# Performance work log

Measured on AMD Instinct MI355X. Metric: run time of the kernel, lower is better.

## Reference

```python
import jax, jax.numpy as jnp
import numpy as np


def setup_inputs() -> dict:
    key = jax.random.key(0)
    k1, k2 = jax.random.split(key)
    B, T, D = 16, 512, 256
    feats = jax.random.normal(k1, (B, T, D), dtype=jnp.float32)
    hidden = jax.random.normal(k2, (B, T, 2 * D), dtype=jnp.float32)
    return {"feats": feats, "hidden": hidden, "seq_len": T}


def reference(feats, hidden, seq_len):
    # feats: (B, T, D); hidden: (B, T, 2D); all sequences have length seq_len == T
    B, T, D = feats.shape
    zero = jnp.zeros((B, 1, D), dtype=feats.dtype)
    # X_fw layout per sequence: [feat_0..feat_{T-1}, 0]; X_bw: [0, feat_0..feat_{T-1}]
    X_fw = jnp.concatenate([feats, zero], axis=1).reshape(B * (T + 1), D)
    X_bw = jnp.concatenate([zero, feats], axis=1).reshape(B * (T + 1), D)

    h_fw = hidden[..., :D]  # (B, T, D) forward LSTM half
    h_bw = hidden[..., D:]  # (B, T, D) backward LSTM half

    # (B, T, N) with N = B*(T+1): full softmax over every token slot (as original)
    fw_lp = jax.nn.log_softmax(jnp.einsum('btd,nd->btn', h_fw, X_fw), axis=-1)
    bw_lp = jax.nn.log_softmax(jnp.einsum('btd,nd->btn', h_bw, X_bw), axis=-1)

    t = jnp.arange(T)
    # original takes diag of columns [1:1+T] (fw) and [0:T] (bw) for EVERY sequence
    fw_diag = fw_lp[:, t, t + 1]  # (B, T)
    bw_diag = bw_lp[:, t, t]      # (B, T)

    fw_loss = (-fw_diag.sum(axis=1) / seq_len).sum() / B
    bw_loss = (-bw_diag.sum(axis=1) / seq_len).sum() / B
    return fw_loss, bw_loss
```

## Files before the change

### kernel.cpp

```cpp
#include <hip/hip_runtime.h>
#include <hip/hip_bf16.h>
#include <stdint.h>

typedef int   int32x4 __attribute__((ext_vector_type(4)));
typedef float floatx4 __attribute__((ext_vector_type(4)));

#define D      256
#define TLEN   512
#define BATCH  16
#define NQ     16384
#define NK     8192
#define BN     64
#define KS     16
#define NTILE  (NK / BN)
#define TPS    (NTILE / KS)
#define TILE_BYTES (BN * D)
#define MSHIFT 64.0f
#define QSCALE 32.0f
#define SSCALE 11818.5577f
#define SMAGIC 1065095716.0f
#define LOG2E  1.4426950408889634f

__device__ __forceinline__ int q8(float x) {
    float y = x * QSCALE;
    y = fminf(fmaxf(y, -127.f), 127.f);
    return (int)rintf(y);
}

__device__ __forceinline__ void quant16(const float* __restrict__ src,
                                        int32x4* __restrict__ dst, int i) {
    const float4* s4 = reinterpret_cast<const float4*>(src) + (size_t)i * 4;
    int32x4 o;
    #pragma unroll
    for (int j = 0; j < 4; ++j) {
        float4 v = s4[j];
        o[j] = (q8(v.x) & 255) | ((q8(v.y) & 255) << 8) |
               ((q8(v.z) & 255) << 16) | ((q8(v.w) & 255) << 24);
    }
    dst[i] = o;
}

__global__ void prep_kernel(const float* __restrict__ feats,
                            const float* __restrict__ hidden,
                            int32x4* __restrict__ Qi8, int32x4* __restrict__ Ki8,
                            float* __restrict__ tfw, float* __restrict__ tbw) {
    int b = blockIdx.x;
    if (b < 1024) {
        quant16(hidden, Qi8, b * 256 + threadIdx.x);
        return;
    }
    if (b < 1536) {
        quant16(feats, Ki8, (b - 1024) * 256 + threadIdx.x);
        return;
    }
    int gw   = (b - 1536) * 4 + (threadIdx.x >> 6);
    int lane = threadIdx.x & 63;
    int t = gw & (TLEN - 1);
    const float4* h4 = reinterpret_cast<const float4*>(hidden + (size_t)gw * (2 * D));
    float sfw = 0.f, sbw = 0.f;
    if (t < TLEN - 1) {
        const float4* f4 = reinterpret_cast<const float4*>(feats + (size_t)(t + 1) * D);
        float4 x = h4[lane], y = f4[lane];
        sfw = x.x * y.x + x.y * y.y + x.z * y.z + x.w * y.w;
    }
    if (t > 0) {
        const float4* f4 = reinterpret_cast<const float4*>(feats + (size_t)(t - 1) * D);
        float4 x = h4[64 + lane], y = f4[lane];
        sbw = x.x * y.x + x.y * y.y + x.z * y.z + x.w * y.w;
    }
    #pragma unroll
    for (int mask = 32; mask > 0; mask >>= 1) {
        sfw += __shfl_xor(sfw, mask);
        sbw += __shfl_xor(sbw, mask);
    }
    if (lane == 0) { tfw[gw] = sfw; tbw[gw] = sbw; }
}

__global__ __launch_bounds__(512, 2) void lse_kernel(const char* __restrict__ Qi8,
                                                     const char* __restrict__ Ki8,
                                                     float* __restrict__ ps) {
    const int qblk  = blockIdx.x >> 4;
    const int slice = blockIdx.x & 15;
    const int q0    = qblk * 512;
    const int tid   = threadIdx.x;
    const int wave  = tid >> 6;
    const int lane  = tid & 63;
    const int lrow  = lane & 15;
    const int lgrp  = lane >> 4;

    __shared__ __align__(16) char Klds[2][BN * D];

    int32x4 a[4][4];
    #pragma unroll
    for (int mf = 0; mf < 4; ++mf) {
        const char* qbase = Qi8 + (size_t)(q0 + wave * 64 + mf * 16 + lrow) * D + lgrp * 16;
        #pragma unroll
        for (int s = 0; s < 4; ++s)
            a[mf][s] = *reinterpret_cast<const int32x4*>(qbase + s * 64);
    }

    int voff[4];
    #pragma unroll
    for (int s = 0; s < 4; ++s)
        voff[s] = lrow * 256 + ((((s * 4 + lgrp) ^ (lrow & 7))) * 16);

    int soff[2];
    #pragma unroll
    for (int i = 0; i < 2; ++i) {
        int cl  = tid + i * 512;
        int row = cl >> 4, c = cl & 15;
        soff[i] = (row * 16 + (c ^ (row & 7))) * 16;
    }

    const char* ksrc = Ki8 + (size_t)(slice * TPS) * TILE_BYTES;

    auto issue = [&](int buf, int t) {
        const char* tb = ksrc + (size_t)t * TILE_BYTES;
        #pragma unroll
        for (int i = 0; i < 2; ++i) {
            const char* gp = tb + soff[i];
            char* lp = (char*)(&Klds[0][0]) + buf * 16384 + (i * 512 + wave * 64) * 16;
            __builtin_amdgcn_global_load_lds(
                (const __attribute__((address_space(1))) void*)gp,
                (__attribute__((address_space(3))) void*)lp,
                16, 0, 0);
        }
    };

    float srun[4][4];
    #pragma unroll
    for (int mf = 0; mf < 4; ++mf)
        #pragma unroll
        for (int r = 0; r < 4; ++r) srun[mf][r] = 0.f;

    auto compute = [&](int buf) {
        const char* kb = (const char*)(&Klds[0][0]) + buf * 16384;
        #pragma unroll
        for (int sub = 0; sub < 4; ++sub) {
            int32x4 c[4];
            #pragma unroll
            for (int mf = 0; mf < 4; ++mf)
                c[mf] = (int32x4){-65536, -65536, -65536, -65536};
            __builtin_amdgcn_s_setprio(1);
            #pragma unroll
            for (int s = 0; s < 4; ++s) {
                int32x4 bfr = *reinterpret_cast<const int32x4*>(kb + voff[s] + sub * 4096);
                #pragma unroll
                for (int mf = 0; mf < 4; ++mf)
                    c[mf] = __builtin_amdgcn_mfma_i32_16x16x64_i8(a[mf][s], bfr, c[mf], 0, 0, 0);
            }
            __builtin_amdgcn_s_setprio(0);
            #pragma unroll
            for (int mf = 0; mf < 4; ++mf)
                #pragma unroll
                for (int r = 0; r < 4; ++r) {
                    float f = (float)c[mf][r];
                    float tt = fmaf(f, SSCALE, SMAGIC);
                    uint32_t u = (uint32_t)tt;
                    srun[mf][r] += __uint_as_float(u);
                }
        }
    };

    issue(0, 0);

    #pragma unroll 1
    for (int t = 0; t < TPS; t += 2) {
        asm volatile("s_waitcnt vmcnt(0)" ::: "memory");
        __builtin_amdgcn_s_barrier();
        asm volatile("" ::: "memory");
        issue(1, t + 1);
        compute(0);
        asm volatile("s_waitcnt vmcnt(0)" ::: "memory");
        __builtin_amdgcn_s_barrier();
        asm volatile("" ::: "memory");
        if (t + 2 < TPS) issue(0, t + 2);
        compute(1);
    }

    #pragma unroll
    for (int mf = 0; mf < 4; ++mf)
        #pragma unroll
        for (int r = 0; r < 4; ++r) {
            float v = srun[mf][r];
            v += __shfl_xor(v, 1);
            v += __shfl_xor(v, 2);
            v += __shfl_xor(v, 4);
            v += __shfl_xor(v, 8);
            if (lrow == 0) {
                int q = q0 + wave * 64 + mf * 16 + lgrp * 4 + r;
                ps[slice * NQ + q] = v;
            }
        }
}

__global__ void reduce1_kernel(const float* __restrict__ ps,
                               const float* __restrict__ tfw, const float* __restrict__ tbw,
                               float* __restrict__ partial) {
    __shared__ float red0[256], red1[256];
    int tid = threadIdx.x;
    int i   = blockIdx.x * 256 + tid;
    const float Z16 = 16.f * __expf(-MSHIFT);
    int qf = 2 * i, qb = 2 * i + 1;
    float sfw = Z16, sbw = Z16;
    #pragma unroll
    for (int sl = 0; sl < KS; ++sl) {
        sfw += ps[sl * NQ + qf];
        sbw += ps[sl * NQ + qb];
    }
    float lsef = MSHIFT + logf(sfw);
    float lseb = MSHIFT + logf(sbw);
    red0[tid] = lsef - tfw[i];
    red1[tid] = lseb - tbw[i];
    __syncthreads();
    for (int s2 = 128; s2 > 0; s2 >>= 1) {
        if (tid < s2) { red0[tid] += red0[tid + s2]; red1[tid] += red1[tid + s2]; }
        __syncthreads();
    }
    if (tid == 0) {
        partial[blockIdx.x * 2 + 0] = red0[0];
        partial[blockIdx.x * 2 + 1] = red1[0];
    }
}

__global__ void reduce2_kernel(const float* __restrict__ partial, float* __restrict__ out) {
    int lane = threadIdx.x & 63;
    float fw = (lane < 32) ? partial[lane * 2 + 0] : 0.f;
    float bw = (lane < 32) ? partial[lane * 2 + 1] : 0.f;
    #pragma unroll
    for (int mask = 32; mask > 0; mask >>= 1) {
        fw += __shfl_xor(fw, mask);
        bw += __shfl_xor(bw, mask);
    }
    if (lane == 0) {
        const float denom = (float)TLEN * (float)BATCH;
        out[0] = fw / denom;
        out[1] = bw / denom;
    }
}

extern "C" void kernel_launch(void* const* d_in, const int* in_sizes, int n_in,
                              void* d_out, int out_size, void* d_ws, size_t ws_size,
                              hipStream_t stream) {
    const float* feats  = (const float*)d_in[0];
    const float* hidden = (const float*)d_in[1];
    float* out = (float*)d_out;

    char* ws = (char*)d_ws;
    char*  Qi8  = ws;
    char*  Ki8  = ws + (size_t)NQ * D;
    float* psv  = (float*)(ws + (size_t)NQ * D + (size_t)NK * D);
    float* tfw  = psv + (size_t)KS * NQ;
    float* tbw  = tfw + NK;
    float* part = tbw + NK;

    prep_kernel<<<3584, 256, 0, stream>>>(feats, hidden,
                                          (int32x4*)Qi8, (int32x4*)Ki8, tfw, tbw);

    lse_kernel<<<(NQ / 512) * KS, 512, 0, stream>>>(Qi8, Ki8, psv);

    reduce1_kernel<<<NK / 256, 256, 0, stream>>>(psv, tfw, tbw, part);
    reduce2_kernel<<<1, 64, 0, stream>>>(part, out);
}
```

Baseline: 61.37 us.

## Load int8 key fragments directly from global into registers, dropping LDS staging

The LSE kernel no longer stages key tiles through double-buffered LDS with global_load_lds and barriers. Each wave now loads its B-fragments straight from global memory into two register sets, prefetching the next subtile while the current one runs MFMAs. Blocks shrink to 256 threads and block IDs are remapped across slices. The exp2 bit trick also switches from a biased accumulator init to a new magic constant clamped at zero. The intent is to remove LDS traffic and barrier stalls, at the cost of redundant per-wave global/L2 reads of the same keys.

```diff
diff --git a/kernel.cpp b/kernel.cpp
--- a/kernel.cpp
+++ b/kernel.cpp
@@ -3,23 +3,19 @@
 #include <stdint.h>
 
 typedef int   int32x4 __attribute__((ext_vector_type(4)));
-typedef float floatx4 __attribute__((ext_vector_type(4)));
 
 #define D      256
 #define TLEN   512
 #define BATCH  16
 #define NQ     16384
 #define NK     8192
-#define BN     64
 #define KS     16
-#define NTILE  (NK / BN)
-#define TPS    (NTILE / KS)
-#define TILE_BYTES (BN * D)
+#define SLICE_KEYS (NK / KS)
+#define NSUB   (SLICE_KEYS / 16)
 #define MSHIFT 64.0f
 #define QSCALE 32.0f
-#define SSCALE 11818.5577f
-#define SMAGIC 1065095716.0f
-#define LOG2E  1.4426950408889634f
+#define SSCALE  11818.5577749f
+#define SMAGIC2 290554713.0f
 
 __device__ __forceinline__ int q8(float x) {
     float y = x * QSCALE;
@@ -76,19 +72,18 @@
     if (lane == 0) { tfw[gw] = sfw; tbw[gw] = sbw; }
 }
 
-__global__ __launch_bounds__(512, 2) void lse_kernel(const char* __restrict__ Qi8,
-                                                     const char* __restrict__ Ki8,
-                                                     float* __restrict__ ps) {
-    const int qblk  = blockIdx.x >> 4;
-    const int slice = blockIdx.x & 15;
-    const int q0    = qblk * 512;
-    const int tid   = threadIdx.x;
-    const int wave  = tid >> 6;
-    const int lane  = tid & 63;
+__global__ __launch_bounds__(256) void lse_kernel(const char* __restrict__ Qi8,
+                                                  const char* __restrict__ Ki8,
+                                                  float* __restrict__ ps) {
+    const int bid   = (int)blockIdx.x;
+    const int nbid  = (bid & 7) * 128 + (bid >> 3);
+    const int slice = nbid >> 6;
+    const int qblk  = nbid & 63;
+    const int q0    = qblk * 256;
+    const int wave  = (int)(threadIdx.x >> 6);
+    const int lane  = (int)(threadIdx.x & 63);
     const int lrow  = lane & 15;
     const int lgrp  = lane >> 4;
-
-    __shared__ __align__(16) char Klds[2][BN * D];
 
     int32x4 a[4][4];
     #pragma unroll
@@ -99,33 +94,7 @@
             a[mf][s] = *reinterpret_cast<const int32x4*>(qbase + s * 64);
     }
 
-    int voff[4];
-    #pragma unroll
-    for (int s = 0; s < 4; ++s)
-        voff[s] = lrow * 256 + ((((s * 4 + lgrp) ^ (lrow & 7))) * 16);
-
-    int soff[2];
-    #pragma unroll
-    for (int i = 0; i < 2; ++i) {
-        int cl  = tid + i * 512;
-        int row = cl >> 4, c = cl & 15;
-        soff[i] = (row * 16 + (c ^ (row & 7))) * 16;
-    }
-
-    const char* ksrc = Ki8 + (size_t)(slice * TPS) * TILE_BYTES;
-
-    auto issue = [&](int buf, int t) {
-        const char* tb = ksrc + (size_t)t * TILE_BYTES;
-        #pragma unroll
-        for (int i = 0; i < 2; ++i) {
-            const char* gp = tb + soff[i];
-            char* lp = (char*)(&Klds[0][0]) + buf * 16384 + (i * 512 + wave * 64) * 16;
-            __builtin_amdgcn_global_load_lds(
-                (const __attribute__((address_space(1))) void*)gp,
-                (__attribute__((address_space(3))) void*)lp,
-                16, 0, 0);
-        }
-    };
+    const char* kp = Ki8 + (size_t)slice * (SLICE_KEYS * D) + lrow * D + lgrp * 16;
 
     float srun[4][4];
     #pragma unroll
@@ -133,49 +102,60 @@
         #pragma unroll
         for (int r = 0; r < 4; ++r) srun[mf][r] = 0.f;
 
-    auto compute = [&](int buf) {
-        const char* kb = (const char*)(&Klds[0][0]) + buf * 16384;
-        #pragma unroll
-        for (int sub = 0; sub < 4; ++sub) {
+    int32x4 bA[4], bB[4];
+    #pragma unroll
+    for (int s = 0; s < 4; ++s) {
+        bA[s] = *reinterpret_cast<const int32x4*>(kp + s * 64);
+        bB[s] = *reinterpret_cast<const int32x4*>(kp + 4096 + s * 64);
+    }
+
+    #pragma unroll 1
+    for (int j = 0; j < NSUB; j += 2) {
+        const char* pA = kp + (size_t)((j + 2 < NSUB) ? j + 2 : 0) * 4096;
+        const char* pB = kp + (size_t)((j + 3 < NSUB) ? j + 3 : 1) * 4096;
+
+        {
             int32x4 c[4];
             #pragma unroll
-            for (int mf = 0; mf < 4; ++mf)
-                c[mf] = (int32x4){-65536, -65536, -65536, -65536};
-            __builtin_amdgcn_s_setprio(1);
-            #pragma unroll
-            for (int s = 0; s < 4; ++s) {
-                int32x4 bfr = *reinterpret_cast<const int32x4*>(kb + voff[s] + sub * 4096);
+            for (int mf = 0; mf < 4; ++mf) c[mf] = (int32x4){0, 0, 0, 0};
+            #pragma unroll
+            for (int s = 0; s < 4; ++s)
                 #pragma unroll
                 for (int mf = 0; mf < 4; ++mf)
-                    c[mf] = __builtin_amdgcn_mfma_i32_16x16x64_i8(a[mf][s], bfr, c[mf], 0, 0, 0);
-            }
-            __builtin_amdgcn_s_setprio(0);
+                    c[mf] = __builtin_amdgcn_mfma_i32_16x16x64_i8(a[mf][s], bA[s], c[mf], 0, 0, 0);
+            #pragma unroll
+            for (int s = 0; s < 4; ++s)
+                bA[s] = *reinterpret_cast<const int32x4*>(pA + s * 64);
             #pragma unroll
             for (int mf = 0; mf < 4; ++mf)
                 #pragma unroll
                 for (int r = 0; r < 4; ++r) {
                     float f = (float)c[mf][r];
-                    float tt = fmaf(f, SSCALE, SMAGIC);
-                    uint32_t u = (uint32_t)tt;
-                    srun[mf][r] += __uint_as_float(u);
+                    float tt = fmaxf(fmaf(f, SSCALE, SMAGIC2), 0.f);
+                    srun[mf][r] += __uint_as_float((uint32_t)tt);
                 }
         }
-    };
-
-    issue(0, 0);
-
-    #pragma unroll 1
-    for (int t = 0; t < TPS; t += 2) {
-        asm volatile("s_waitcnt vmcnt(0)" ::: "memory");
-        __builtin_amdgcn_s_barrier();
-        asm volatile("" ::: "memory");
-        issue(1, t + 1);
-        compute(0);
-        asm volatile("s_waitcnt vmcnt(0)" ::: "memory");
-        __builtin_amdgcn_s_barrier();
-        asm volatile("" ::: "memory");
-        if (t + 2 < TPS) issue(0, t + 2);
-        compute(1);
+        {
+            int32x4 c[4];
+            #pragma unroll
+            for (int mf = 0; mf < 4; ++mf) c[mf] = (int32x4){0, 0, 0, 0};
+            #pragma unroll
+            for (int s = 0; s < 4; ++s)
+                #pragma unroll
+                for (int mf = 0; mf < 4; ++mf)
+                    c[mf] = __builtin_amdgcn_mfma_i32_16x16x64_i8(a[mf][s], bB[s], c[mf], 0, 0, 0);
+            #pragma unroll
+            for (int s = 0; s < 4; ++s)
+                bB[s] = *reinterpret_cast<const int32x4*>(pB + s * 64);
+            #pragma unroll
+            for (int mf = 0; mf < 4; ++mf)
+                #pragma unroll
+                for (int r = 0; r < 4; ++r) {
+                    float f = (float)c[mf][r];
+                    float tt = fmaxf(fmaf(f, SSCALE, SMAGIC2), 0.f);
+                    srun[mf][r] += __uint_as_float((uint32_t)tt);
+                }
+        }
     }
 
     #pragma unroll
@@ -257,7 +237,7 @@
     prep_kernel<<<3584, 256, 0, stream>>>(feats, hidden,
                                           (int32x4*)Qi8, (int32x4*)Ki8, tfw, tbw);
 
-    lse_kernel<<<(NQ / 512) * KS, 512, 0, stream>>>(Qi8, Ki8, psv);
+    lse_kernel<<<(NQ / 256) * KS, 256, 0, stream>>>(Qi8, Ki8, psv);
 
     reduce1_kernel<<<NK / 256, 256, 0, stream>>>(psv, tfw, tbw, part);
     reduce2_kernel<<<1, 64, 0, stream>>>(part, out);
```

Result: slower. 88.97 us (+45.0%).
